# Kernel tuning notes

Hardware: AMD Instinct MI355X
Metric: run time of the kernel (lower is better)

Reference implementation:

```python
import jax, jax.numpy as jnp
import numpy as np

N_OUT = 8      # outer experts
INNER = 2      # inner experts per outer expert
E = N_OUT * INNER  # 16 total experts
ACTI = 2       # outer top-k (acti_num)
PATTERN = (2, 1)   # inner top-k per outer slot (acti_pattern)
D = 1024       # hidden_dim
F = 512        # expert ffn dim
B, S = 1, 1024


def setup_inputs() -> dict:
    key = jax.random.key(0)
    ks = jax.random.split(key, 6)
    w = lambda k, shape: jax.random.normal(k, shape, jnp.float32) * 0.02
    return {
        "hidden_states": jax.random.normal(ks[0], (B, S, D), jnp.float32),
        "w_out_gate": w(ks[1], (N_OUT, D)),
        "w_in_gates": w(ks[2], (N_OUT, INNER, D)),
        "w_gate_proj": w(ks[3], (E, F, D)),
        "w_up_proj": w(ks[4], (E, F, D)),
        "w_down_proj": w(ks[5], (E, D, F)),
    }


def reference(hidden_states, w_out_gate, w_in_gates, w_gate_proj, w_up_proj, w_down_proj):
    Bb, Ss, Dd = hidden_states.shape
    x = hidden_states.reshape(-1, Dd)          # [T, D]
    T = x.shape[0]

    # --- RouterCompound: outer gate ---
    logits = x @ w_out_gate.T                  # [T, n_out]
    probs = jax.nn.softmax(logits.astype(jnp.float32), axis=-1)
    rw, sel = jax.lax.top_k(probs, ACTI)       # [T, A] weights, outer expert ids
    rw = rw / rw.sum(axis=-1, keepdims=True)   # norm_topk_prob=True

    # --- inner gates: score all (outer, inner) pairs, gather selected outer ---
    inner_all = jnp.einsum('td,oid->toi', x, w_in_gates)           # [T, n_out, inner]
    inner_sel = jnp.take_along_axis(inner_all, sel[:, :, None], axis=1)  # [T, A, inner]
    max_k = max(PATTERN)
    _, top_idx = jax.lax.top_k(inner_sel, max_k)                   # [T, A, max_k]
    flat_ids = sel[:, :, None] * INNER + top_idx                   # global expert ids
    # per outer slot j keep first PATTERN[j] inner experts (static pattern)
    sel_ids = jnp.concatenate([flat_ids[:, j, :p] for j, p in enumerate(PATTERN)], axis=1)  # [T, K]
    sel_w = jnp.concatenate([jnp.repeat(rw[:, j:j + 1], p, axis=1) for j, p in enumerate(PATTERN)], axis=1)  # [T, K]
    sel_w = sel_w.astype(x.dtype)

    # --- dispatch/combine: dense masked combine (math-identical to index_add loop) ---
    combine = jnp.zeros((T, E), x.dtype).at[jnp.arange(T)[:, None], sel_ids].add(sel_w)  # [T, E]
    g = jnp.einsum('td,efd->tef', x, w_gate_proj)   # [T, E, F]
    u = jnp.einsum('td,efd->tef', x, w_up_proj)
    h = jax.nn.silu(g) * u                          # SwiGLU activation
    y = jnp.einsum('tef,edf->ted', h, w_down_proj)  # [T, E, D]
    out = jnp.einsum('ted,te->td', y, combine)      # weighted combine
    return out.reshape(Bb, Ss, Dd), sel_w
```

## Files before the change

kernel.cpp:

```cpp
#include <hip/hip_runtime.h>
#include <hip/hip_bf16.h>

typedef __bf16 bf16_t;
typedef __bf16 bf16x8 __attribute__((ext_vector_type(8)));
typedef float floatx4 __attribute__((ext_vector_type(4)));
typedef unsigned int u32;

#define T_TOK 1024
#define DIM   1024
#define FF    512
#define NEXP  16

#define FLAG_OFF 0
#define CNT_OFF  64
#define TOK_OFF  256
#define SEL_OFF  65792
#define H_OFF    78080
#define XBF_OFF  (H_OFF + (size_t)3072*512*2)
#define WGB_OFF  (XBF_OFF + (size_t)T_TOK*DIM*2)
#define WUB_OFF  (WGB_OFF + (size_t)NEXP*FF*DIM*2)
#define WDB_OFF  (WUB_OFF + (size_t)NEXP*FF*DIM*2)
#define Y_OFF    (WDB_OFF + (size_t)NEXP*DIM*FF*2)
#define WS_FULL  (Y_OFF + (size_t)3072*DIM*4)

__device__ inline float swiglu(float g, float u) {
    float a = fminf(fmaxf(-g, -60.f), 60.f);
    return g * u / (1.0f + __expf(a));
}

__device__ __forceinline__ void gload_lds16(const void* g, void* l) {
    __builtin_amdgcn_global_load_lds((const __attribute__((address_space(1))) u32*)g,
                                     (__attribute__((address_space(3))) u32*)l, 16, 0, 0);
}

__device__ __forceinline__ bf16x8 cvt8(float4 a, float4 b) {
    bf16x8 r;
    r[0]=(bf16_t)a.x; r[1]=(bf16_t)a.y; r[2]=(bf16_t)a.z; r[3]=(bf16_t)a.w;
    r[4]=(bf16_t)b.x; r[5]=(bf16_t)b.y; r[6]=(bf16_t)b.z; r[7]=(bf16_t)b.w;
    return r;
}

__device__ __forceinline__ bf16x8 rd128(const bf16_t* L, int row, int q) {
    return *(const bf16x8*)(L + row * 128 + ((q ^ (row & 15)) << 3));
}

__global__ __launch_bounds__(64) void detect_kernel(
    const void* p0, const void* p1, const void* p2,
    const void* p3, const void* p4, const void* p5,
    int* __restrict__ flags)
{
    const void* ps[6] = {p0, p1, p2, p3, p4, p5};
    int j = blockIdx.x;
    int lane = threadIdx.x;
    const unsigned short* h = (const unsigned short*)ps[j];
    unsigned int bad = 0;
    for (int i = lane; i < 4096; i += 64) {
        unsigned int e = ((unsigned int)h[i] >> 7) & 0xFFu;
        if (e >= 0x90u) bad = 1;
    }
    unsigned long long b = __ballot(bad);
    if (lane == 0) flags[j] = (b != 0ull) ? 1 : 0;
}

__global__ __launch_bounds__(256) void wcvt_kernel(
    const void* __restrict__ wg, const void* __restrict__ wu, const void* __restrict__ wd,
    const int* __restrict__ flags,
    bf16_t* __restrict__ gb, bf16_t* __restrict__ ub, bf16_t* __restrict__ db)
{
    const int z = blockIdx.y;
    const void* src; bf16_t* dst; int f;
    if (z == 0)      { src = wg; dst = gb; f = flags[3]; }
    else if (z == 1) { src = wu; dst = ub; f = flags[4]; }
    else             { src = wd; dst = db; f = flags[5]; }
    if (!f) return;
    size_t i = ((size_t)blockIdx.x * 256 + threadIdx.x) * 8;
    const float4* p = (const float4*)((const float*)src + i);
    float4 a = p[0], b = p[1];
    *(bf16x8*)(dst + i) = cvt8(a, b);
}

__device__ inline bf16x8 loadB8r(const void* base, size_t off, bool f32) {
    if (f32) {
        const float4* p = (const float4*)((const float*)base + off);
        float4 v0 = p[0], v1 = p[1];
        return cvt8(v0, v1);
    } else {
        return *(const bf16x8*)((const bf16_t*)base + off);
    }
}

__global__ __launch_bounds__(256) void router3_kernel(
    const void* __restrict__ x,
    const void* __restrict__ w_out,
    const void* __restrict__ w_in,
    float* __restrict__ selw_out,
    const int* __restrict__ flags,
    int* __restrict__ sel_ids,
    bf16_t* __restrict__ xb)
{
    const bool xf  = flags[0] != 0;
    const bool gof = flags[1] != 0;
    const bool gif = flags[2] != 0;
    const int tid = threadIdx.x;
    const int wave = tid >> 6, lane = tid & 63;
    const int t = blockIdx.x;

    __shared__ float Ls[24];

    float xv[16];
    if (xf) {
        const float* xp = (const float*)x + (size_t)t * DIM;
        #pragma unroll
        for (int i = 0; i < 16; i++) xv[i] = xp[lane + 64 * i];
    } else {
        const bf16_t* xp = (const bf16_t*)x + (size_t)t * DIM;
        #pragma unroll
        for (int i = 0; i < 16; i++) xv[i] = (float)xp[lane + 64 * i];
    }

    if (wave == 0 && xb) {
        #pragma unroll
        for (int i = 0; i < 16; i++)
            xb[(size_t)t * DIM + lane + 64 * i] = (bf16_t)xv[i];
    }

    #pragma unroll
    for (int jj = 0; jj < 6; jj++) {
        const int j = wave * 6 + jj;
        const void* gb; int row; bool gf;
        if (j < 8) { gb = w_out; row = j;     gf = gof; }
        else       { gb = w_in;  row = j - 8; gf = gif; }
        float s = 0.f;
        if (gf) {
            const float* gp = (const float*)gb + (size_t)row * DIM;
            #pragma unroll
            for (int i = 0; i < 16; i++) s += xv[i] * gp[lane + 64 * i];
        } else {
            const bf16_t* gp = (const bf16_t*)gb + (size_t)row * DIM;
            #pragma unroll
            for (int i = 0; i < 16; i++) s += xv[i] * (float)gp[lane + 64 * i];
        }
        #pragma unroll
        for (int m = 32; m >= 1; m >>= 1) s += __shfl_xor(s, m, 64);
        if (lane == 0) Ls[j] = s;
    }
    __syncthreads();

    if (tid == 0) {
        const float* logits = Ls;
        float mx = logits[0];
        for (int o = 1; o < 8; o++) mx = fmaxf(mx, logits[o]);
        float p[8];
        for (int o = 0; o < 8; o++) p[o] = __expf(logits[o] - mx);
        int i0 = 0;
        for (int o = 1; o < 8; o++) if (logits[o] > logits[i0]) i0 = o;
        int i1 = (i0 == 0) ? 1 : 0;
        for (int o = 0; o < 8; o++) if (o != i0 && logits[o] > logits[i1]) i1 = o;
        float rsum = p[i0] + p[i1];
        float rw0 = p[i0] / rsum, rw1 = p[i1] / rsum;

        float a0 = logits[8 + i0 * 2], a1 = logits[8 + i0 * 2 + 1];
        int j00 = (a1 > a0) ? 1 : 0;
        float b0 = logits[8 + i1 * 2], b1 = logits[8 + i1 * 2 + 1];
        int j10 = (b1 > b0) ? 1 : 0;

        int   ids[3] = { i0 * 2 + j00, i0 * 2 + (1 - j00), i1 * 2 + j10 };
        float w[3]   = { rw0, rw0, rw1 };

        #pragma unroll
        for (int k = 0; k < 3; k++) {
            selw_out[t * 3 + k] = w[k];
            sel_ids[t * 3 + k]  = ids[k];
        }
    }
}

__global__ __launch_bounds__(1024) void bin2_kernel(
    const int* __restrict__ sel_ids,
    int* __restrict__ cnt, int* __restrict__ tok_enc)
{
    const int e = blockIdx.x, tid = threadIdx.x;
    const int wave = tid >> 6, lane = tid & 63;
    __shared__ int wbase[16];

    int my = -1;
    #pragma unroll
    for (int k = 0; k < 3; k++) {
        int id = sel_ids[tid * 3 + k];
        if (id == e) my = tid | (k << 16);
    }
    unsigned long long b = __ballot(my >= 0);
    if (lane == 0) wbase[wave] = __popcll(b);
    __syncthreads();
    if (tid == 0) {
        int s = 0;
        for (int w = 0; w < 16; w++) { int c = wbase[w]; wbase[w] = s; s += c; }
        cnt[e] = s;
    }
    __syncthreads();
    if (my >= 0) {
        int pos = wbase[wave] + __popcll(b & ((1ull << lane) - 1ull));
        if (pos < T_TOK) tok_enc[e * T_TOK + pos] = my;
    }
}


__global__ __launch_bounds__(512, 1) void gateup3_kernel(
    const bf16_t* __restrict__ xb,
    const void* __restrict__ wg, const void* __restrict__ wu,
    const bf16_t* __restrict__ wgb, const bf16_t* __restrict__ wub,
    const int* __restrict__ flags, const int* __restrict__ cnt,
    const int* __restrict__ tok_enc, bf16_t* __restrict__ H)
{
    __shared__ __align__(16) bf16_t Xs[2][128 * 128];
    __shared__ __align__(16) bf16_t Gs[2][64 * 128];
    __shared__ __align__(16) bf16_t Us[2][64 * 128];
    __shared__ int toks[128];
    __shared__ int hrow[128];

    const int ft = blockIdx.x, mt = blockIdx.y, e = blockIdx.z;
    int C = cnt[e]; if (C > T_TOK) C = T_TOK; if (C < 0) C = 0;
    if (mt * 128 >= C) return;

    const bf16_t* wgp = (flags[3] != 0) ? wgb : (const bf16_t*)wg;
    const bf16_t* wup = (flags[4] != 0) ? wub : (const bf16_t*)wu;

    const int tid = threadIdx.x;
    if (tid < 128) {
        int idx = mt * 128 + tid, t = 0, hr = -1;
        if (idx < C) {
            int enc = tok_enc[e * T_TOK + idx];
            int tt = enc & 0xFFFF, kk = (enc >> 16) & 0xFFFF;
            if (tt < T_TOK && kk < 3) { t = tt; hr = tt * 3 + kk; }
        }
        toks[tid] = t; hrow[tid] = hr;
    }
    __syncthreads();

    const int wave = tid >> 6, lane = tid & 63;
    const int mh = wave >> 2, fq = wave & 3;
    const int rsel = lane & 15, kq = lane >> 4;

    const bf16_t* sx[4];
    #pragma unroll
    for (int j = 0; j < 4; j++) {
        int n = (j * 8 + wave) * 64 + lane, r = n >> 4, s = n & 15;
        sx[j] = xb + (size_t)toks[r] * DIM + ((s ^ (r & 15)) << 3);
    }
    const bf16_t* sg[2]; const bf16_t* su[2];
    #pragma unroll
    for (int j = 0; j < 2; j++) {
        int n = (j * 8 + wave) * 64 + lane, r = n >> 4, s = n & 15;
        size_t off = (size_t)(e * FF + ft * 64 + r) * DIM + ((s ^ (r & 15)) << 3);
        sg[j] = wgp + off; su[j] = wup + off;
    }

    #pragma unroll
    for (int j = 0; j < 4; j++) gload_lds16(sx[j], &Xs[0][(j * 8 + wave) * 512]);
    #pragma unroll
    for (int j = 0; j < 2; j++) gload_lds16(sg[j], &Gs[0][(j * 8 + wave) * 512]);
    #pragma unroll
    for (int j = 0; j < 2; j++) gload_lds16(su[j], &Us[0][(j * 8 + wave) * 512]);

    floatx4 ag[4], au[4];
    #pragma unroll
    for (int ms = 0; ms < 4; ms++) { ag[ms] = (floatx4){0,0,0,0}; au[ms] = (floatx4){0,0,0,0}; }

    __syncthreads();

    for (int kc = 0; kc < 8; kc++) {
        if (kc < 7) {
            const int b = (kc + 1) & 1, ko = (kc + 1) * 128;
            #pragma unroll
            for (int j = 0; j < 4; j++) gload_lds16(sx[j] + ko, &Xs[b][(j * 8 + wave) * 512]);
            #pragma unroll
            for (int j = 0; j < 2; j++) gload_lds16(sg[j] + ko, &Gs[b][(j * 8 + wave) * 512]);
            #pragma unroll
            for (int j = 0; j < 2; j++) gload_lds16(su[j] + ko, &Us[b][(j * 8 + wave) * 512]);
        }
        const bf16_t* X = Xs[kc & 1];
        const bf16_t* G = Gs[kc & 1];
        const bf16_t* U = Us[kc & 1];
        #pragma unroll
        for (int i = 0; i < 4; i++) {
            const int q = i * 4 + kq;
            bf16x8 a[4];
            #pragma unroll
            for (int ms = 0; ms < 4; ms++) a[ms] = rd128(X, mh * 64 + ms * 16 + rsel, q);
            bf16x8 bg = rd128(G, fq * 16 + rsel, q);
            bf16x8 bu = rd128(U, fq * 16 + rsel, q);
            #pragma unroll
            for (int ms = 0; ms < 4; ms++) {
                ag[ms] = __builtin_amdgcn_mfma_f32_16x16x32_bf16(a[ms], bg, ag[ms], 0, 0, 0);
                au[ms] = __builtin_amdgcn_mfma_f32_16x16x32_bf16(a[ms], bu, au[ms], 0, 0, 0);
            }
        }
        __syncthreads();
    }

    const int f = ft * 64 + fq * 16 + rsel;
    #pragma unroll
    for (int ms = 0; ms < 4; ms++)
        #pragma unroll
        for (int r = 0; r < 4; r++) {
            int m = mh * 64 + ms * 16 + kq * 4 + r;
            int hr = hrow[m];
            if (hr >= 0)
                H[(size_t)hr * FF + f] = (bf16_t)swiglu(ag[ms][r], au[ms][r]);
        }
}

__global__ __launch_bounds__(512, 1) void down3_kernel(
    const void* __restrict__ wd, const bf16_t* __restrict__ wdb,
    const int* __restrict__ flags, const int* __restrict__ cnt,
    const int* __restrict__ tok_enc, const bf16_t* __restrict__ H,
    float* __restrict__ Y)
{
    __shared__ __align__(16) bf16_t Hs[2][128 * 128];
    __shared__ __align__(16) bf16_t Ds[2][128 * 128];
    __shared__ int hsrc[128];
    __shared__ int hdst[128];

    const int dt = blockIdx.x, mt = blockIdx.y, e = blockIdx.z;
    int C = cnt[e]; if (C > T_TOK) C = T_TOK; if (C < 0) C = 0;
    if (mt * 128 >= C) return;

    const bf16_t* wdp = (flags[5] != 0) ? wdb : (const bf16_t*)wd;

    const int tid = threadIdx.x;
    if (tid < 128) {
        int idx = mt * 128 + tid, hr = -1;
        if (idx < C) {
            int enc = tok_enc[e * T_TOK + idx];
            int tt = enc & 0xFFFF, kk = (enc >> 16) & 0xFFFF;
            if (tt < T_TOK && kk < 3) hr = tt * 3 + kk;
        }
        hsrc[tid] = (hr >= 0) ? hr : 0;
        hdst[tid] = hr;
    }
    __syncthreads();

    const int wave = tid >> 6, lane = tid & 63;
    const int mh = wave >> 2, dq = wave & 3;
    const int rsel = lane & 15, kq = lane >> 4;

    const bf16_t* sh[4]; const bf16_t* sd[4];
    #pragma unroll
    for (int j = 0; j < 4; j++) {
        int n = (j * 8 + wave) * 64 + lane, r = n >> 4, s = n & 15;
        sh[j] = H + (size_t)hsrc[r] * FF + ((s ^ (r & 15)) << 3);
        sd[j] = wdp + (size_t)(e * DIM + dt * 128 + r) * FF + ((s ^ (r & 15)) << 3);
    }

    #pragma unroll
    for (int j = 0; j < 4; j++) gload_lds16(sh[j], &Hs[0][(j * 8 + wave) * 512]);
    #pragma unroll
    for (int j = 0; j < 4; j++) gload_lds16(sd[j], &Ds[0][(j * 8 + wave) * 512]);

    floatx4 acc[4][2];
    #pragma unroll
    for (int ms = 0; ms < 4; ms++)
        #pragma unroll
        for (int nt = 0; nt < 2; nt++) acc[ms][nt] = (floatx4){0,0,0,0};

    __syncthreads();

    for (int kc = 0; kc < 4; kc++) {
        if (kc < 3) {
            const int b = (kc + 1) & 1, ko = (kc + 1) * 128;
            #pragma unroll
            for (int j = 0; j < 4; j++) gload_lds16(sh[j] + ko, &Hs[b][(j * 8 + wave) * 512]);
            #pragma unroll
            for (int j = 0; j < 4; j++) gload_lds16(sd[j] + ko, &Ds[b][(j * 8 + wave) * 512]);
        }
        const bf16_t* Hb = Hs[kc & 1];
        const bf16_t* Db = Ds[kc & 1];
        #pragma unroll
        for (int i = 0; i < 4; i++) {
            const int q = i * 4 + kq;
            bf16x8 a[4], bd[2];
            #pragma unroll
            for (int ms = 0; ms < 4; ms++) a[ms] = rd128(Hb, mh * 64 + ms * 16 + rsel, q);
            #pragma unroll
            for (int nt = 0; nt < 2; nt++) bd[nt] = rd128(Db, dq * 32 + nt * 16 + rsel, q);
            #pragma unroll
            for (int ms = 0; ms < 4; ms++)
                #pragma unroll
                for (int nt = 0; nt < 2; nt++)
                    acc[ms][nt] = __builtin_amdgcn_mfma_f32_16x16x32_bf16(a[ms], bd[nt], acc[ms][nt], 0, 0, 0);
        }
        __syncthreads();
    }

    #pragma unroll
    for (int ms = 0; ms < 4; ms++)
        #pragma unroll
        for (int nt = 0; nt < 2; nt++)
            #pragma unroll
            for (int r = 0; r < 4; r++) {
                int m = mh * 64 + ms * 16 + kq * 4 + r;
                int hr = hdst[m];
                if (hr >= 0)
                    Y[(size_t)hr * DIM + dt * 128 + dq * 32 + nt * 16 + rsel] = acc[ms][nt][r];
            }
}

__global__ __launch_bounds__(256) void combine_kernel(
    const float* __restrict__ Y, const float* __restrict__ selw,
    float* __restrict__ outp)
{
    int idx = blockIdx.x * 256 + threadIdx.x;
    int t = idx >> 8;
    int d = (idx & 255) * 4;
    float w0 = selw[t * 3 + 0], w1 = selw[t * 3 + 1], w2 = selw[t * 3 + 2];
    float4 y0 = *(const float4*)(Y + (size_t)(t * 3 + 0) * DIM + d);
    float4 y1 = *(const float4*)(Y + (size_t)(t * 3 + 1) * DIM + d);
    float4 y2 = *(const float4*)(Y + (size_t)(t * 3 + 2) * DIM + d);
    float4 o;
    o.x = w0 * y0.x + w1 * y1.x + w2 * y2.x;
    o.y = w0 * y0.y + w1 * y1.y + w2 * y2.y;
    o.z = w0 * y0.z + w1 * y1.z + w2 * y2.z;
    o.w = w0 * y0.w + w1 * y1.w + w2 * y2.w;
    *(float4*)(outp + (size_t)t * DIM + d) = o;
}

__global__ __launch_bounds__(256) void ffn_kernel(
    const void* __restrict__ x,
    const void* __restrict__ wg, const void* __restrict__ wu, const void* __restrict__ wd,
    const int* __restrict__ flags, const int* __restrict__ cnt, const int* __restrict__ tok_enc,
    const float* __restrict__ selw, float* __restrict__ outp)
{
    const int e = blockIdx.x, tile = blockIdx.y;
    int C = cnt[e]; if (C > T_TOK) C = T_TOK; if (C < 0) C = 0;
    if (tile * 16 >= C) return;
    const bool xf = flags[0] != 0, gf = flags[3] != 0, uf = flags[4] != 0, df = flags[5] != 0;

    __shared__ __align__(16) bf16_t Xs[16][1032];
    __shared__ __align__(16) bf16_t Hs[16][520];
    __shared__ int toks[16];
    __shared__ float wts[16];
    const int tid = threadIdx.x;
    if (tid < 16) {
        int idx = tile * 16 + tid, t = -1; float w = 0.f;
        if (idx < C) {
            int enc = tok_enc[e * T_TOK + idx];
            int tt = enc & 0xFFFF, kk = (enc >> 16) & 0xFFFF;
            if (tt < T_TOK && kk < 3) { t = tt; w = selw[tt * 3 + kk]; }
        }
        toks[tid] = t; wts[tid] = w;
    }
    __syncthreads();
    {
        int row = tid >> 4, chunk = tid & 15;
        int t = toks[row];
        bf16x8* dst = (bf16x8*)&Xs[row][chunk * 64];
        if (t >= 0) {
            #pragma unroll
            for (int i = 0; i < 8; i++)
                dst[i] = loadB8r(x, (size_t)t * DIM + chunk * 64 + i * 8, xf);
        } else {
            bf16x8 z;
            #pragma unroll
            for (int kz = 0; kz < 8; kz++) z[kz] = (bf16_t)0.0f;
            #pragma unroll
            for (int i = 0; i < 8; i++) dst[i] = z;
        }
    }
    __syncthreads();

    const int wave = tid >> 6, lane = tid & 63;
    const int rsel = lane & 15, kq = lane >> 4;
    const size_t eoffF = (size_t)e * FF * DIM;
    for (int nt = 0; nt < 8; nt++) {
        const int f0 = wave * 128 + nt * 16;
        const size_t boff = eoffF + (size_t)(f0 + rsel) * DIM + kq * 8;
        const bf16_t* ap = &Xs[rsel][kq * 8];
        floatx4 accg = {0.f,0.f,0.f,0.f};
        floatx4 accu = {0.f,0.f,0.f,0.f};
        for (int k0 = 0; k0 < DIM; k0 += 32) {
            bf16x8 a  = *(const bf16x8*)(ap + k0);
            bf16x8 bg = loadB8r(wg, boff + k0, gf);
            bf16x8 bu = loadB8r(wu, boff + k0, uf);
            accg = __builtin_amdgcn_mfma_f32_16x16x32_bf16(a, bg, accg, 0, 0, 0);
            accu = __builtin_amdgcn_mfma_f32_16x16x32_bf16(a, bu, accu, 0, 0, 0);
        }
        #pragma unroll
        for (int r = 0; r < 4; r++)
            Hs[kq * 4 + r][f0 + rsel] = (bf16_t)swiglu(accg[r], accu[r]);
    }
    __syncthreads();
    const size_t eoffD = (size_t)e * DIM * FF;
    for (int nt = 0; nt < 16; nt++) {
        const int d0 = wave * 256 + nt * 16;
        const size_t boff = eoffD + (size_t)(d0 + rsel) * FF + kq * 8;
        const bf16_t* ap = &Hs[rsel][kq * 8];
        floatx4 acc = {0.f,0.f,0.f,0.f};
        for (int k0 = 0; k0 < FF; k0 += 32) {
            bf16x8 a = *(const bf16x8*)(ap + k0);
            bf16x8 b = loadB8r(wd, boff + k0, df);
            acc = __builtin_amdgcn_mfma_f32_16x16x32_bf16(a, b, acc, 0, 0, 0);
        }
        #pragma unroll
        for (int r = 0; r < 4; r++) {
            int m = kq * 4 + r, t = toks[m];
            if (t >= 0) atomicAdd(outp + (size_t)t * DIM + d0 + rsel, acc[r] * wts[m]);
        }
    }
}

extern "C" void kernel_launch(void* const* d_in, const int* in_sizes, int n_in,
                              void* d_out, int out_size, void* d_ws, size_t ws_size,
                              hipStream_t stream)
{
    const void* x     = d_in[0];
    const void* w_out = d_in[1];
    const void* w_in  = d_in[2];
    const void* wg    = d_in[3];
    const void* wu    = d_in[4];
    const void* wd    = d_in[5];
    float* out  = (float*)d_out;
    float* selw = out + (size_t)T_TOK * DIM;

    char* ws = (char*)d_ws;
    int*    flags = (int*)(ws + FLAG_OFF);
    int*    cnt   = (int*)(ws + CNT_OFF);
    int*    tok   = (int*)(ws + TOK_OFF);
    int*    sel   = (int*)(ws + SEL_OFF);
    bf16_t* H     = (bf16_t*)(ws + H_OFF);
    bf16_t* xbf   = (bf16_t*)(ws + XBF_OFF);
    bf16_t* wgb   = (bf16_t*)(ws + WGB_OFF);
    bf16_t* wub   = (bf16_t*)(ws + WUB_OFF);
    bf16_t* wdb   = (bf16_t*)(ws + WDB_OFF);
    float*  Y     = (float*)(ws + Y_OFF);

    const bool full = ws_size >= (size_t)WS_FULL;

    detect_kernel<<<dim3(6), dim3(64), 0, stream>>>(x, w_out, w_in, wg, wu, wd, flags);

    if (full) {
        hipMemsetAsync(Y, 0, (size_t)3072 * DIM * sizeof(float), stream);
        wcvt_kernel<<<dim3(4096, 3), dim3(256), 0, stream>>>(wg, wu, wd, flags, wgb, wub, wdb);
    } else {
        hipMemsetAsync(out, 0, (size_t)T_TOK * DIM * sizeof(float), stream);
    }

    router3_kernel<<<dim3(T_TOK), dim3(256), 0, stream>>>(
        x, w_out, w_in, selw, flags, sel, full ? xbf : (bf16_t*)nullptr);

    bin2_kernel<<<dim3(NEXP), dim3(1024), 0, stream>>>(sel, cnt, tok);

    if (full) {
        gateup3_kernel<<<dim3(8, 8, 16), dim3(512), 0, stream>>>(
            xbf, wg, wu, wgb, wub, flags, cnt, tok, H);
        down3_kernel<<<dim3(8, 8, 16), dim3(512), 0, stream>>>(
            wd, wdb, flags, cnt, tok, H, Y);
        combine_kernel<<<dim3(T_TOK * DIM / 1024), dim3(256), 0, stream>>>(Y, selw, out);
    } else {
        ffn_kernel<<<dim3(NEXP, 64), dim3(256), 0, stream>>>(
            x, wg, wu, wd, flags, cnt, tok, selw, out);
    }
}
```

Measured before the change: 215.7 us.

## Convert fp32 expert weights in LDS during GEMM and triple-buffer the k-loop

Drops the separate weight-conversion pass, which wrote bf16 copies of all expert weights. Gate/up and down GEMMs now stream fp32 weights straight into LDS and convert to bf16 when reading fragments, avoiding a full extra read and write of the weights. The k-loop goes from double to triple buffering with smaller k-chunks, using explicit vmcnt waits and raw barriers. Dtype detection is folded into the router kernel and the Y memset is removed, at the cost of redundant per-block detection work and twice the LDS footprint and global load traffic per chunk for fp32 weights.

```diff
diff --git a/kernel.cpp b/kernel.cpp
--- a/kernel.cpp
+++ b/kernel.cpp
@@ -17,10 +17,7 @@
 #define SEL_OFF  65792
 #define H_OFF    78080
 #define XBF_OFF  (H_OFF + (size_t)3072*512*2)
-#define WGB_OFF  (XBF_OFF + (size_t)T_TOK*DIM*2)
-#define WUB_OFF  (WGB_OFF + (size_t)NEXP*FF*DIM*2)
-#define WDB_OFF  (WUB_OFF + (size_t)NEXP*FF*DIM*2)
-#define Y_OFF    (WDB_OFF + (size_t)NEXP*DIM*FF*2)
+#define Y_OFF    (XBF_OFF + (size_t)T_TOK*DIM*2)
 #define WS_FULL  (Y_OFF + (size_t)3072*DIM*4)
 
 __device__ inline float swiglu(float g, float u) {
@@ -32,6 +29,11 @@
     __builtin_amdgcn_global_load_lds((const __attribute__((address_space(1))) u32*)g,
                                      (__attribute__((address_space(3))) u32*)l, 16, 0, 0);
 }
+
+template<int N> __device__ __forceinline__ void waitv() {
+    asm volatile("s_waitcnt vmcnt(%0)" :: "n"(N) : "memory");
+}
+__device__ __forceinline__ void barrier_raw() { __builtin_amdgcn_s_barrier(); }
 
 __device__ __forceinline__ bf16x8 cvt8(float4 a, float4 b) {
     bf16x8 r;
@@ -40,72 +42,77 @@
     return r;
 }
 
-__device__ __forceinline__ bf16x8 rd128(const bf16_t* L, int row, int q) {
-    return *(const bf16x8*)(L + row * 128 + ((q ^ (row & 15)) << 3));
-}
-
-__global__ __launch_bounds__(64) void detect_kernel(
-    const void* p0, const void* p1, const void* p2,
-    const void* p3, const void* p4, const void* p5,
-    int* __restrict__ flags)
-{
-    const void* ps[6] = {p0, p1, p2, p3, p4, p5};
-    int j = blockIdx.x;
-    int lane = threadIdx.x;
-    const unsigned short* h = (const unsigned short*)ps[j];
-    unsigned int bad = 0;
-    for (int i = lane; i < 4096; i += 64) {
-        unsigned int e = ((unsigned int)h[i] >> 7) & 0xFFu;
-        if (e >= 0x90u) bad = 1;
-    }
-    unsigned long long b = __ballot(bad);
-    if (lane == 0) flags[j] = (b != 0ull) ? 1 : 0;
-}
-
-__global__ __launch_bounds__(256) void wcvt_kernel(
-    const void* __restrict__ wg, const void* __restrict__ wu, const void* __restrict__ wd,
-    const int* __restrict__ flags,
-    bf16_t* __restrict__ gb, bf16_t* __restrict__ ub, bf16_t* __restrict__ db)
-{
-    const int z = blockIdx.y;
-    const void* src; bf16_t* dst; int f;
-    if (z == 0)      { src = wg; dst = gb; f = flags[3]; }
-    else if (z == 1) { src = wu; dst = ub; f = flags[4]; }
-    else             { src = wd; dst = db; f = flags[5]; }
-    if (!f) return;
-    size_t i = ((size_t)blockIdx.x * 256 + threadIdx.x) * 8;
-    const float4* p = (const float4*)((const float*)src + i);
-    float4 a = p[0], b = p[1];
-    *(bf16x8*)(dst + i) = cvt8(a, b);
+__device__ __forceinline__ bf16x8 rdA(const char* L, int r, int q) {
+    return *(const bf16x8*)(L + r * 128 + ((q ^ (r & 7)) << 4));
+}
+template<bool F32>
+__device__ __forceinline__ bf16x8 rdB(const char* L, int r, int q) {
+    if constexpr (F32) {
+        const float* p = (const float*)(L + r * 256);
+        float4 a = *(const float4*)(p + ((((2*q)    ) ^ (r & 15)) << 2));
+        float4 b = *(const float4*)(p + ((((2*q) + 1) ^ (r & 15)) << 2));
+        return cvt8(a, b);
+    } else {
+        return *(const bf16x8*)(L + r * 128 + ((q ^ (r & 7)) << 4));
+    }
 }
 
 __device__ inline bf16x8 loadB8r(const void* base, size_t off, bool f32) {
     if (f32) {
         const float4* p = (const float4*)((const float*)base + off);
-        float4 v0 = p[0], v1 = p[1];
-        return cvt8(v0, v1);
+        return cvt8(p[0], p[1]);
     } else {
         return *(const bf16x8*)((const bf16_t*)base + off);
     }
 }
 
-__global__ __launch_bounds__(256) void router3_kernel(
-    const void* __restrict__ x,
-    const void* __restrict__ w_out,
-    const void* __restrict__ w_in,
-    float* __restrict__ selw_out,
-    const int* __restrict__ flags,
-    int* __restrict__ sel_ids,
-    bf16_t* __restrict__ xb)
-{
-    const bool xf  = flags[0] != 0;
-    const bool gof = flags[1] != 0;
-    const bool gif = flags[2] != 0;
+__device__ int blk_f32(const void* p, int tid, int* tmp) {
+    const unsigned short* h = (const unsigned short*)p;
+    unsigned bad = 0;
+    for (int i = tid; i < 4096; i += 256) {
+        unsigned e = ((unsigned)h[i] >> 7) & 0xFFu;
+        if (e >= 0x90u) bad = 1;
+    }
+    unsigned long long bl = __ballot(bad != 0);
+    __syncthreads();
+    if ((tid & 63) == 0) tmp[tid >> 6] = (bl != 0ull) ? 1 : 0;
+    __syncthreads();
+    return tmp[0] | tmp[1] | tmp[2] | tmp[3];
+}
+
+__global__ __launch_bounds__(256) void prep_kernel(
+    const void* __restrict__ x, const void* __restrict__ w_out, const void* __restrict__ w_in,
+    const void* __restrict__ wg, const void* __restrict__ wu, const void* __restrict__ wd,
+    float* __restrict__ selw_out, int* __restrict__ sel_ids,
+    bf16_t* __restrict__ xb, int* __restrict__ flags)
+{
+    const int b = blockIdx.x;
     const int tid = threadIdx.x;
+    __shared__ int tmp[4];
+    __shared__ float Ls[24];
+
+    if (b >= T_TOK) {
+        const int j = b - T_TOK;
+        const void* ps[6] = {x, w_out, w_in, wg, wu, wd};
+        const unsigned short* h = (const unsigned short*)ps[j];
+        unsigned bad = 0;
+        for (int i = tid; i < 4096; i += 256) {
+            unsigned e = ((unsigned)h[i] >> 7) & 0xFFu;
+            if (e >= 0x90u) bad = 1;
+        }
+        unsigned long long bl = __ballot(bad != 0);
+        if ((tid & 63) == 0) tmp[tid >> 6] = (bl != 0ull) ? 1 : 0;
+        __syncthreads();
+        if (tid == 0) flags[j] = tmp[0] | tmp[1] | tmp[2] | tmp[3];
+        return;
+    }
+
+    const bool xf  = blk_f32(x, tid, tmp) != 0;
+    const bool gof = blk_f32(w_out, tid, tmp) != 0;
+    const bool gif = blk_f32(w_in, tid, tmp) != 0;
+
     const int wave = tid >> 6, lane = tid & 63;
-    const int t = blockIdx.x;
-
-    __shared__ float Ls[24];
+    const int t = b;
 
     float xv[16];
     if (xf) {
@@ -205,25 +212,17 @@
 }
 
 
-__global__ __launch_bounds__(512, 1) void gateup3_kernel(
+template<bool GF, bool UF>
+__device__ __forceinline__ void gateup4_body(
     const bf16_t* __restrict__ xb,
     const void* __restrict__ wg, const void* __restrict__ wu,
-    const bf16_t* __restrict__ wgb, const bf16_t* __restrict__ wub,
-    const int* __restrict__ flags, const int* __restrict__ cnt,
-    const int* __restrict__ tok_enc, bf16_t* __restrict__ H)
-{
-    __shared__ __align__(16) bf16_t Xs[2][128 * 128];
-    __shared__ __align__(16) bf16_t Gs[2][64 * 128];
-    __shared__ __align__(16) bf16_t Us[2][64 * 128];
-    __shared__ int toks[128];
-    __shared__ int hrow[128];
-
+    const int* __restrict__ cnt, const int* __restrict__ tok_enc,
+    bf16_t* __restrict__ H,
+    char* Xs, char* Gs, char* Us, int* toks, int* hrow)
+{
     const int ft = blockIdx.x, mt = blockIdx.y, e = blockIdx.z;
     int C = cnt[e]; if (C > T_TOK) C = T_TOK; if (C < 0) C = 0;
     if (mt * 128 >= C) return;
-
-    const bf16_t* wgp = (flags[3] != 0) ? wgb : (const bf16_t*)wg;
-    const bf16_t* wup = (flags[4] != 0) ? wub : (const bf16_t*)wu;
 
     const int tid = threadIdx.x;
     if (tid < 128) {
@@ -241,61 +240,98 @@
     const int mh = wave >> 2, fq = wave & 3;
     const int rsel = lane & 15, kq = lane >> 4;
 
-    const bf16_t* sx[4];
-    #pragma unroll
-    for (int j = 0; j < 4; j++) {
-        int n = (j * 8 + wave) * 64 + lane, r = n >> 4, s = n & 15;
-        sx[j] = xb + (size_t)toks[r] * DIM + ((s ^ (r & 15)) << 3);
-    }
-    const bf16_t* sg[2]; const bf16_t* su[2];
+    constexpr int NC  = 16;
+    constexpr int NG  = GF ? 2 : 1;
+    constexpr int NU  = UF ? 2 : 1;
+    constexpr int PER = 2 + NG + NU;
+    constexpr int GSTR = GF ? 16384 : 8192;
+    constexpr int USTR = UF ? 16384 : 8192;
+    const int wrow0 = e * FF + ft * 64;
+
+    const bf16_t* px[2];
     #pragma unroll
     for (int j = 0; j < 2; j++) {
-        int n = (j * 8 + wave) * 64 + lane, r = n >> 4, s = n & 15;
-        size_t off = (size_t)(e * FF + ft * 64 + r) * DIM + ((s ^ (r & 15)) << 3);
-        sg[j] = wgp + off; su[j] = wup + off;
-    }
-
-    #pragma unroll
-    for (int j = 0; j < 4; j++) gload_lds16(sx[j], &Xs[0][(j * 8 + wave) * 512]);
-    #pragma unroll
-    for (int j = 0; j < 2; j++) gload_lds16(sg[j], &Gs[0][(j * 8 + wave) * 512]);
-    #pragma unroll
-    for (int j = 0; j < 2; j++) gload_lds16(su[j], &Us[0][(j * 8 + wave) * 512]);
+        int n = (j * 8 + wave) * 64 + lane, r = n >> 3, s = n & 7;
+        px[j] = xb + (size_t)toks[r] * DIM + ((s ^ (r & 7)) << 3);
+    }
+    const float*  pgf[2]; const bf16_t* pgh = nullptr;
+    const float*  puf[2]; const bf16_t* puh = nullptr;
+    if constexpr (GF) {
+        #pragma unroll
+        for (int j = 0; j < 2; j++) {
+            int n = (j * 8 + wave) * 64 + lane, r = n >> 4, s = n & 15;
+            pgf[j] = (const float*)wg + (size_t)(wrow0 + r) * DIM + ((s ^ (r & 15)) << 2);
+        }
+    } else {
+        int n = wave * 64 + lane, r = n >> 3, s = n & 7;
+        pgh = (const bf16_t*)wg + (size_t)(wrow0 + r) * DIM + ((s ^ (r & 7)) << 3);
+    }
+    if constexpr (UF) {
+        #pragma unroll
+        for (int j = 0; j < 2; j++) {
+            int n = (j * 8 + wave) * 64 + lane, r = n >> 4, s = n & 15;
+            puf[j] = (const float*)wu + (size_t)(wrow0 + r) * DIM + ((s ^ (r & 15)) << 2);
+        }
+    } else {
+        int n = wave * 64 + lane, r = n >> 3, s = n & 7;
+        puh = (const bf16_t*)wu + (size_t)(wrow0 + r) * DIM + ((s ^ (r & 7)) << 3);
+    }
+
+    auto issue = [&](int kc) {
+        const int buf = kc % 3;
+        #pragma unroll
+        for (int j = 0; j < 2; j++)
+            gload_lds16(px[j] + kc * 64, Xs + buf * 16384 + (j * 8 + wave) * 1024);
+        if constexpr (GF) {
+            #pragma unroll
+            for (int j = 0; j < 2; j++)
+                gload_lds16(pgf[j] + kc * 64, Gs + buf * GSTR + (j * 8 + wave) * 1024);
+        } else {
+            gload_lds16(pgh + kc * 64, Gs + buf * GSTR + wave * 1024);
+        }
+        if constexpr (UF) {
+            #pragma unroll
+            for (int j = 0; j < 2; j++)
+                gload_lds16(puf[j] + kc * 64, Us + buf * USTR + (j * 8 + wave) * 1024);
+        } else {
+            gload_lds16(puh + kc * 64, Us + buf * USTR + wave * 1024);
+        }
+    };
 
     floatx4 ag[4], au[4];
     #pragma unroll
     for (int ms = 0; ms < 4; ms++) { ag[ms] = (floatx4){0,0,0,0}; au[ms] = (floatx4){0,0,0,0}; }
 
-    __syncthreads();
-
-    for (int kc = 0; kc < 8; kc++) {
-        if (kc < 7) {
-            const int b = (kc + 1) & 1, ko = (kc + 1) * 128;
-            #pragma unroll
-            for (int j = 0; j < 4; j++) gload_lds16(sx[j] + ko, &Xs[b][(j * 8 + wave) * 512]);
-            #pragma unroll
-            for (int j = 0; j < 2; j++) gload_lds16(sg[j] + ko, &Gs[b][(j * 8 + wave) * 512]);
-            #pragma unroll
-            for (int j = 0; j < 2; j++) gload_lds16(su[j] + ko, &Us[b][(j * 8 + wave) * 512]);
-        }
-        const bf16_t* X = Xs[kc & 1];
-        const bf16_t* G = Gs[kc & 1];
-        const bf16_t* U = Us[kc & 1];
-        #pragma unroll
-        for (int i = 0; i < 4; i++) {
+    issue(0);
+    issue(1);
+
+    #pragma unroll
+    for (int kc = 0; kc < NC; kc++) {
+        if (kc + 2 < NC) issue(kc + 2);
+        if (kc + 2 < NC)      waitv<2 * PER>();
+        else if (kc + 1 < NC) waitv<PER>();
+        else                  waitv<0>();
+        barrier_raw();
+        __builtin_amdgcn_sched_barrier(0);
+
+        const char* X = Xs + (kc % 3) * 16384;
+        const char* G = Gs + (kc % 3) * GSTR;
+        const char* U = Us + (kc % 3) * USTR;
+        #pragma unroll
+        for (int i = 0; i < 2; i++) {
             const int q = i * 4 + kq;
             bf16x8 a[4];
             #pragma unroll
-            for (int ms = 0; ms < 4; ms++) a[ms] = rd128(X, mh * 64 + ms * 16 + rsel, q);
-            bf16x8 bg = rd128(G, fq * 16 + rsel, q);
-            bf16x8 bu = rd128(U, fq * 16 + rsel, q);
+            for (int ms = 0; ms < 4; ms++) a[ms] = rdA(X, mh * 64 + ms * 16 + rsel, q);
+            bf16x8 bg = rdB<GF>(G, fq * 16 + rsel, q);
+            bf16x8 bu = rdB<UF>(U, fq * 16 + rsel, q);
             #pragma unroll
             for (int ms = 0; ms < 4; ms++) {
                 ag[ms] = __builtin_amdgcn_mfma_f32_16x16x32_bf16(a[ms], bg, ag[ms], 0, 0, 0);
                 au[ms] = __builtin_amdgcn_mfma_f32_16x16x32_bf16(a[ms], bu, au[ms], 0, 0, 0);
             }
         }
-        __syncthreads();
+        barrier_raw();
     }
 
     const int f = ft * 64 + fq * 16 + rsel;
@@ -310,22 +346,37 @@
         }
 }
 
-__global__ __launch_bounds__(512, 1) void down3_kernel(
-    const void* __restrict__ wd, const bf16_t* __restrict__ wdb,
+__global__ __launch_bounds__(512, 1) void gateup4_kernel(
+    const bf16_t* __restrict__ xb,
+    const void* __restrict__ wg, const void* __restrict__ wu,
     const int* __restrict__ flags, const int* __restrict__ cnt,
-    const int* __restrict__ tok_enc, const bf16_t* __restrict__ H,
-    float* __restrict__ Y)
-{
-    __shared__ __align__(16) bf16_t Hs[2][128 * 128];
-    __shared__ __align__(16) bf16_t Ds[2][128 * 128];
-    __shared__ int hsrc[128];
-    __shared__ int hdst[128];
-
+    const int* __restrict__ tok_enc, bf16_t* __restrict__ H)
+{
+    __shared__ __align__(16) char Xs[3 * 16384];
+    __shared__ __align__(16) char Gs[3 * 16384];
+    __shared__ __align__(16) char Us[3 * 16384];
+    __shared__ int toks[128];
+    __shared__ int hrow[128];
+    const bool gf = flags[3] != 0, uf = flags[4] != 0;
+    if (gf) {
+        if (uf) gateup4_body<true,  true >(xb, wg, wu, cnt, tok_enc, H, Xs, Gs, Us, toks, hrow);
+        else    gateup4_body<true,  false>(xb, wg, wu, cnt, tok_enc, H, Xs, Gs, Us, toks, hrow);
+    } else {
+        if (uf) gateup4_body<false, true >(xb, wg, wu, cnt, tok_enc, H, Xs, Gs, Us, toks, hrow);
+        else    gateup4_body<false, false>(xb, wg, wu, cnt, tok_enc, H, Xs, Gs, Us, toks, hrow);
+    }
+}
+
+template<bool DF>
+__device__ __forceinline__ void down4_body(
+    const void* __restrict__ wd,
+    const int* __restrict__ cnt, const int* __restrict__ tok_enc,
+    const bf16_t* __restrict__ H, float* __restrict__ Y,
+    char* Hs, char* Ds, int* hsrc, int* hdst)
+{
     const int dt = blockIdx.x, mt = blockIdx.y, e = blockIdx.z;
     int C = cnt[e]; if (C > T_TOK) C = T_TOK; if (C < 0) C = 0;
     if (mt * 128 >= C) return;
-
-    const bf16_t* wdp = (flags[5] != 0) ? wdb : (const bf16_t*)wd;
 
     const int tid = threadIdx.x;
     if (tid < 128) {
@@ -344,18 +395,48 @@
     const int mh = wave >> 2, dq = wave & 3;
     const int rsel = lane & 15, kq = lane >> 4;
 
-    const bf16_t* sh[4]; const bf16_t* sd[4];
-    #pragma unroll
-    for (int j = 0; j < 4; j++) {
-        int n = (j * 8 + wave) * 64 + lane, r = n >> 4, s = n & 15;
-        sh[j] = H + (size_t)hsrc[r] * FF + ((s ^ (r & 15)) << 3);
-        sd[j] = wdp + (size_t)(e * DIM + dt * 128 + r) * FF + ((s ^ (r & 15)) << 3);
-    }
-
-    #pragma unroll
-    for (int j = 0; j < 4; j++) gload_lds16(sh[j], &Hs[0][(j * 8 + wave) * 512]);
-    #pragma unroll
-    for (int j = 0; j < 4; j++) gload_lds16(sd[j], &Ds[0][(j * 8 + wave) * 512]);
+    constexpr int NC  = 8;
+    constexpr int ND  = DF ? 4 : 2;
+    constexpr int PER = 2 + ND;
+    constexpr int DSTR = DF ? 32768 : 16384;
+    const int wrow0 = e * DIM + dt * 128;
+
+    const bf16_t* ph[2];
+    #pragma unroll
+    for (int j = 0; j < 2; j++) {
+        int n = (j * 8 + wave) * 64 + lane, r = n >> 3, s = n & 7;
+        ph[j] = H + (size_t)hsrc[r] * FF + ((s ^ (r & 7)) << 3);
+    }
+    const float*  pdf[4]; const bf16_t* pdh[2];
+    if constexpr (DF) {
+        #pragma unroll
+        for (int j = 0; j < 4; j++) {
+            int n = (j * 8 + wave) * 64 + lane, r = n >> 4, s = n & 15;
+            pdf[j] = (const float*)wd + (size_t)(wrow0 + r) * FF + ((s ^ (r & 15)) << 2);
+        }
+    } else {
+        #pragma unroll
+        for (int j = 0; j < 2; j++) {
+            int n = (j * 8 + wave) * 64 + lane, r = n >> 3, s = n & 7;
+            pdh[j] = (const bf16_t*)wd + (size_t)(wrow0 + r) * FF + ((s ^ (r & 7)) << 3);
+        }
+    }
+
+    auto issue = [&](int kc) {
+        const int buf = kc % 3;
+        #pragma unroll
+        for (int j = 0; j < 2; j++)
+            gload_lds16(ph[j] + kc * 64, Hs + buf * 16384 + (j * 8 + wave) * 1024);
+        if constexpr (DF) {
+            #pragma unroll
+            for (int j = 0; j < 4; j++)
+                gload_lds16(pdf[j] + kc * 64, Ds + buf * DSTR + (j * 8 + wave) * 1024);
+        } else {
+            #pragma unroll
+            for (int j = 0; j < 2; j++)
+                gload_lds16(pdh[j] + kc * 64, Ds + buf * DSTR + (j * 8 + wave) * 1024);
+        }
+    };
 
     floatx4 acc[4][2];
     #pragma unroll
@@ -363,33 +444,35 @@
         #pragma unroll
         for (int nt = 0; nt < 2; nt++) acc[ms][nt] = (floatx4){0,0,0,0};
 
-    __syncthreads();
-
-    for (int kc = 0; kc < 4; kc++) {
-        if (kc < 3) {
-            const int b = (kc + 1) & 1, ko = (kc + 1) * 128;
-            #pragma unroll
-            for (int j = 0; j < 4; j++) gload_lds16(sh[j] + ko, &Hs[b][(j * 8 + wave) * 512]);
-            #pragma unroll
-            for (int j = 0; j < 4; j++) gload_lds16(sd[j] + ko, &Ds[b][(j * 8 + wave) * 512]);
-        }
-        const bf16_t* Hb = Hs[kc & 1];
-        const bf16_t* Db = Ds[kc & 1];
-        #pragma unroll
-        for (int i = 0; i < 4; i++) {
+    issue(0);
+    issue(1);
+
+    #pragma unroll
+    for (int kc = 0; kc < NC; kc++) {
+        if (kc + 2 < NC) issue(kc + 2);
+        if (kc + 2 < NC)      waitv<2 * PER>();
+        else if (kc + 1 < NC) waitv<PER>();
+        else                  waitv<0>();
+        barrier_raw();
+        __builtin_amdgcn_sched_barrier(0);
+
+        const char* Hb = Hs + (kc % 3) * 16384;
+        const char* Db = Ds + (kc % 3) * DSTR;
+        #pragma unroll
+        for (int i = 0; i < 2; i++) {
             const int q = i * 4 + kq;
             bf16x8 a[4], bd[2];
             #pragma unroll
-            for (int ms = 0; ms < 4; ms++) a[ms] = rd128(Hb, mh * 64 + ms * 16 + rsel, q);
-            #pragma unroll
-            for (int nt = 0; nt < 2; nt++) bd[nt] = rd128(Db, dq * 32 + nt * 16 + rsel, q);
+            for (int ms = 0; ms < 4; ms++) a[ms] = rdA(Hb, mh * 64 + ms * 16 + rsel, q);
+            #pragma unroll
+            for (int nt = 0; nt < 2; nt++) bd[nt] = rdB<DF>(Db, dq * 32 + nt * 16 + rsel, q);
             #pragma unroll
             for (int ms = 0; ms < 4; ms++)
                 #pragma unroll
                 for (int nt = 0; nt < 2; nt++)
                     acc[ms][nt] = __builtin_amdgcn_mfma_f32_16x16x32_bf16(a[ms], bd[nt], acc[ms][nt], 0, 0, 0);
         }
-        __syncthreads();
+        barrier_raw();
     }
 
     #pragma unroll
@@ -403,6 +486,21 @@
                 if (hr >= 0)
                     Y[(size_t)hr * DIM + dt * 128 + dq * 32 + nt * 16 + rsel] = acc[ms][nt][r];
             }
+}
+
+__global__ __launch_bounds__(512, 1) void down4_kernel(
+    const void* __restrict__ wd,
+    const int* __restrict__ flags, const int* __restrict__ cnt,
+    const int* __restrict__ tok_enc,
+    const bf16_t* __restrict__ H, float* __restrict__ Y)
+{
+    __shared__ __align__(16) char Hs[3 * 16384];
+    __shared__ __align__(16) char Ds[3 * 32768];
+    __shared__ int hsrc[128];
+    __shared__ int hdst[128];
+    const bool df = flags[5] != 0;
+    if (df) down4_body<true >(wd, cnt, tok_enc, H, Y, Hs, Ds, hsrc, hdst);
+    else    down4_body<false>(wd, cnt, tok_enc, H, Y, Hs, Ds, hsrc, hdst);
 }
 
 __global__ __launch_bounds__(256) void combine_kernel(
@@ -528,32 +626,23 @@
     int*    sel   = (int*)(ws + SEL_OFF);
     bf16_t* H     = (bf16_t*)(ws + H_OFF);
     bf16_t* xbf   = (bf16_t*)(ws + XBF_OFF);
-    bf16_t* wgb   = (bf16_t*)(ws + WGB_OFF);
-    bf16_t* wub   = (bf16_t*)(ws + WUB_OFF);
-    bf16_t* wdb   = (bf16_t*)(ws + WDB_OFF);
     float*  Y     = (float*)(ws + Y_OFF);
 
     const bool full = ws_size >= (size_t)WS_FULL;
 
-    detect_kernel<<<dim3(6), dim3(64), 0, stream>>>(x, w_out, w_in, wg, wu, wd, flags);
+    if (!full)
+        hipMemsetAsync(out, 0, (size_t)T_TOK * DIM * sizeof(float), stream);
+
+    prep_kernel<<<dim3(T_TOK + 6), dim3(256), 0, stream>>>(
+        x, w_out, w_in, wg, wu, wd, selw, sel, full ? xbf : (bf16_t*)nullptr, flags);
+
+    bin2_kernel<<<dim3(NEXP), dim3(1024), 0, stream>>>(sel, cnt, tok);
 
     if (full) {
-        hipMemsetAsync(Y, 0, (size_t)3072 * DIM * sizeof(float), stream);
-        wcvt_kernel<<<dim3(4096, 3), dim3(256), 0, stream>>>(wg, wu, wd, flags, wgb, wub, wdb);
-    } else {
-        hipMemsetAsync(out, 0, (size_t)T_TOK * DIM * sizeof(float), stream);
-    }
-
-    router3_kernel<<<dim3(T_TOK), dim3(256), 0, stream>>>(
-        x, w_out, w_in, selw, flags, sel, full ? xbf : (bf16_t*)nullptr);
-
-    bin2_kernel<<<dim3(NEXP), dim3(1024), 0, stream>>>(sel, cnt, tok);
-
-    if (full) {
-        gateup3_kernel<<<dim3(8, 8, 16), dim3(512), 0, stream>>>(
-            xbf, wg, wu, wgb, wub, flags, cnt, tok, H);
-        down3_kernel<<<dim3(8, 8, 16), dim3(512), 0, stream>>>(
-            wd, wdb, flags, cnt, tok, H, Y);
+        gateup4_kernel<<<dim3(8, 8, 16), dim3(512), 0, stream>>>(
+            xbf, wg, wu, flags, cnt, tok, H);
+        down4_kernel<<<dim3(8, 8, 16), dim3(512), 0, stream>>>(
+            wd, flags, cnt, tok, H, Y);
         combine_kernel<<<dim3(T_TOK * DIM / 1024), dim3(256), 0, stream>>>(Y, selw, out);
     } else {
         ffn_kernel<<<dim3(NEXP, 64), dim3(256), 0, stream>>>(
```

After: 201.5 us. -6.6%, faster.
